# Optimization experiments

Hardware: AMD Instinct MI355X
Metric: run time of the kernel (lower is better)

## Reference

```python
import jax, jax.numpy as jnp
import numpy as np

STRIDES = (8, 16, 32, 64, 128)
NUM_CLASSES = 80
TOPK = 1000
CONF_THRESH = 0.05
NMS_THRESH = 0.6
IMG_H = IMG_W = 2048
CLASS_OFFSET = 100000.0  # > any box coordinate, makes different-class boxes disjoint


def _level_decode(cls, reg, ctn, scale, stride):
    # cls: [1,C,H,W], reg: [1,4,H,W], ctn: [1,1,H,W]
    C, H, W = cls.shape[1], cls.shape[2], cls.shape[3]
    cls = jnp.transpose(cls[0], (1, 2, 0)).reshape(-1, C)       # [HW, C]
    reg = jnp.transpose(reg[0], (1, 2, 0)).reshape(-1, 4)       # [HW, 4]
    reg = jax.nn.relu(reg * scale) * stride                      # Scale + relu + stride
    ctn = jnp.transpose(ctn[0], (1, 2, 0)).reshape(-1, 1)       # [HW, 1]
    prob = jnp.sqrt(jax.nn.sigmoid(cls) * jax.nn.sigmoid(ctn))  # [HW, C]
    scores = prob.max(axis=-1)
    labels = prob.argmax(axis=-1)
    ys, xs = jnp.meshgrid(jnp.arange(H), jnp.arange(W), indexing='ij')
    anchors = (jnp.stack([xs, ys], axis=-1).reshape(-1, 2).astype(cls.dtype) + 0.5) * stride
    if scores.shape[0] > TOPK:
        scores, idx = jax.lax.top_k(scores, TOPK)
        labels, reg, anchors = labels[idx], reg[idx], anchors[idx]
    # decode (l,t,r,b) deltas around anchor centers -> (x1,y1,x2,y2)
    boxes = jnp.concatenate([anchors - reg[:, :2], anchors + reg[:, 2:]], axis=-1)
    return scores, labels, boxes


def _nms_keep(boxes, scores, valid, thresh):
    # Sequential greedy NMS, same math as the numpy loop in RTEFCOS.nms.
    order = jnp.argsort(-jnp.where(valid, scores, -jnp.inf))
    b = boxes[order]
    v = valid[order]
    x1, y1, x2, y2 = b[:, 0], b[:, 1], b[:, 2], b[:, 3]
    areas = (x2 - x1) * (y2 - y1)
    n = b.shape[0]
    pos = jnp.arange(n)

    def body(i, keep):
        xx1 = jnp.maximum(x1[i], x1)
        yy1 = jnp.maximum(y1[i], y1)
        xx2 = jnp.minimum(x2[i], x2)
        yy2 = jnp.minimum(y2[i], y2)
        inter = jnp.maximum(1e-10, xx2 - xx1) * jnp.maximum(1e-10, yy2 - yy1)
        ovr = inter / (areas[i] + areas - inter + 1e-14)
        suppress = (ovr > thresh) & (pos > i) & keep[i]
        return keep & (~suppress)

    keep_sorted = jax.lax.fori_loop(0, n, body, v)
    return jnp.zeros(n, dtype=bool).at[order].set(keep_sorted)


def reference(cls0, reg0, ctn0, cls1, reg1, ctn1, cls2, reg2, ctn2,
              cls3, reg3, ctn3, cls4, reg4, ctn4, scales):
    levels = [(cls0, reg0, ctn0), (cls1, reg1, ctn1), (cls2, reg2, ctn2),
              (cls3, reg3, ctn3), (cls4, reg4, ctn4)]
    all_s, all_l, all_b = [], [], []
    for lv, (c, r, t) in enumerate(levels):
        s, l, b = _level_decode(c, r, t, scales[lv], STRIDES[lv])
        all_s.append(s); all_l.append(l); all_b.append(b)
    scores = jnp.concatenate(all_s)   # [M]
    labels = jnp.concatenate(all_l)   # [M]
    bboxes = jnp.concatenate(all_b)   # [M, 4]
    valid = scores >= CONF_THRESH     # conf filter as mask (static shapes)
    # class-wise NMS via coordinate-offset trick: boxes of different classes
    # never overlap, so one greedy pass == per-class greedy passes.
    boxes_off = bboxes + labels[:, None].astype(bboxes.dtype) * CLASS_OFFSET
    keep = _nms_keep(boxes_off, scores, valid, NMS_THRESH)
    bboxes = bboxes / jnp.array([IMG_W, IMG_H, IMG_W, IMG_H], dtype=bboxes.dtype)
    bboxes = jnp.clip(bboxes, 0.0, 1.0)
    return bboxes, scores, labels, keep


def setup_inputs():
    key = jax.random.key(0)
    ks = jax.random.split(key, len(STRIDES))
    inp = {}
    for lv, stride in enumerate(STRIDES):
        H = IMG_H // stride
        W = IMG_W // stride
        k1, k2, k3 = jax.random.split(ks[lv], 3)
        inp[f"cls{lv}"] = jax.random.normal(k1, (1, NUM_CLASSES, H, W), jnp.float32)
        inp[f"reg{lv}"] = jax.random.uniform(k2, (1, 4, H, W), jnp.float32)
        inp[f"ctn{lv}"] = jax.random.normal(k3, (1, 1, H, W), jnp.float32)
    inp["scales"] = jnp.ones((5,), jnp.float32)
    return inp
```

## Files before the change

### kernel.cpp

```cpp
#include <hip/hip_runtime.h>
#include <math.h>

#define TOTAL_ANCHORS 87296
#define NTOPK 87040
#define NSEL 4256
#define NWORDS 67
#define NPAD   4288
#define MAXROUNDS 4300
#define CANDMAX 8192
#define NBIN 32768
#define NSLAB 8
#define PEND_VEC 3216

__device__ __forceinline__ float sigmoidf_(float x) {
    return 1.0f / (1.0f + expf(-x));
}
__device__ __forceinline__ unsigned int f2s(float f) {
    unsigned int u = __float_as_uint(f);
    return u ^ ((u >> 31) ? 0xFFFFFFFFu : 0x80000000u);
}
__device__ __forceinline__ float s2f(unsigned int k) {
    unsigned int u = (k & 0x80000000u) ? (k ^ 0x80000000u) : ~k;
    return __uint_as_float(u);
}
__device__ __forceinline__ float f4e(const float4& v, int j) {
    return (j == 0) ? v.x : ((j == 1) ? v.y : ((j == 2) ? v.z : v.w));
}
__device__ __forceinline__ void level_of(int g, int& lv, int& base, int& W, int& stride) {
    if (g < 65536)      { lv = 0; base = 0;     W = 256; stride = 8;   }
    else if (g < 81920) { lv = 1; base = 65536; W = 128; stride = 16;  }
    else if (g < 86016) { lv = 2; base = 81920; W = 64;  stride = 32;  }
    else if (g < 87040) { lv = 3; base = 86016; W = 32;  stride = 64;  }
    else                { lv = 4; base = 87040; W = 16;  stride = 128; }
}

struct InPtrs {
    const float* cls[5];
    const float* reg[5];
    const float* ctn[5];
    const float* scales;
};

__global__ __launch_bounds__(256) void cmax_kernel(InPtrs in,
        unsigned long long* __restrict__ cmax2) {
    int t = blockIdx.x * 256 + threadIdx.x;
    int a0 = t * 4;
    if (a0 >= TOTAL_ANCHORS) return;
    int cg = blockIdx.y;
    int lv, base, W, stride;
    level_of(a0, lv, base, W, stride);
    (void)stride;
    int p0 = a0 - base;
    int HW = W * W;
    const float* cls = in.cls[lv];
    float4 ct = *(const float4*)&in.ctn[lv][p0];
    float sct0 = sigmoidf_(ct.x), sct1 = sigmoidf_(ct.y);
    float sct2 = sigmoidf_(ct.z), sct3 = sigmoidf_(ct.w);
    int c0 = cg * 8;
    unsigned long long b0 = 0ull, b1 = 0ull, b2 = 0ull, b3 = 0ull;
    #pragma unroll
    for (int k = 0; k < 8; ++k) {
        float4 v = *(const float4*)&cls[(c0 + k) * HW + p0];
        unsigned long long lbl = (unsigned long long)(255 - (c0 + k));
        unsigned long long k0 = ((unsigned long long)f2s(sqrtf(__fmul_rn(sigmoidf_(v.x), sct0))) << 32) | lbl;
        unsigned long long k1 = ((unsigned long long)f2s(sqrtf(__fmul_rn(sigmoidf_(v.y), sct1))) << 32) | lbl;
        unsigned long long k2 = ((unsigned long long)f2s(sqrtf(__fmul_rn(sigmoidf_(v.z), sct2))) << 32) | lbl;
        unsigned long long k3 = ((unsigned long long)f2s(sqrtf(__fmul_rn(sigmoidf_(v.w), sct3))) << 32) | lbl;
        b0 = (k0 > b0) ? k0 : b0;
        b1 = (k1 > b1) ? k1 : b1;
        b2 = (k2 > b2) ? k2 : b2;
        b3 = (k3 > b3) ? k3 : b3;
    }
    unsigned long long* dst = cmax2 + (size_t)cg * TOTAL_ANCHORS + a0;
    dst[0] = b0; dst[1] = b1; dst[2] = b2; dst[3] = b3;
}

__global__ __launch_bounds__(256) void decode2_kernel(InPtrs in,
        const unsigned long long* __restrict__ cmax2,
        unsigned long long* __restrict__ keys, float* __restrict__ scores,
        int* __restrict__ labels, float4* __restrict__ boxes) {
    int t = blockIdx.x * 256 + threadIdx.x;
    int g0 = t * 4;
    if (g0 >= TOTAL_ANCHORS) return;
    int lv, base, W, stride;
    level_of(g0, lv, base, W, stride);
    int p0 = g0 - base;
    int HW = W * W;
    unsigned long long mk0 = 0ull, mk1 = 0ull, mk2 = 0ull, mk3 = 0ull;
    #pragma unroll
    for (int cg = 0; cg < 10; ++cg) {
        const ulonglong2* s2 = (const ulonglong2*)(cmax2 + (size_t)cg * TOTAL_ANCHORS + g0);
        ulonglong2 va = s2[0], vb = s2[1];
        mk0 = (va.x > mk0) ? va.x : mk0;
        mk1 = (va.y > mk1) ? va.y : mk1;
        mk2 = (vb.x > mk2) ? vb.x : mk2;
        mk3 = (vb.y > mk3) ? vb.y : mk3;
    }
    unsigned long long mk[4] = {mk0, mk1, mk2, mk3};
    float scale = in.scales[lv];
    float fs = (float)stride;
    const float* rg = in.reg[lv];
    float4 rq0 = *(const float4*)&rg[0 * HW + p0];
    float4 rq1 = *(const float4*)&rg[1 * HW + p0];
    float4 rq2 = *(const float4*)&rg[2 * HW + p0];
    float4 rq3 = *(const float4*)&rg[3 * HW + p0];
    float4 sc4;
    int4 lb4;
    #pragma unroll
    for (int j = 0; j < 4; ++j) {
        int p = p0 + j;
        int x = p & (W - 1);
        int y = p / W;
        float best = s2f((unsigned int)(mk[j] >> 32));
        int lbl = 255 - (int)(mk[j] & 0xFFull);
        float r0 = __fmul_rn(fmaxf(__fmul_rn(f4e(rq0, j), scale), 0.0f), fs);
        float r1 = __fmul_rn(fmaxf(__fmul_rn(f4e(rq1, j), scale), 0.0f), fs);
        float r2 = __fmul_rn(fmaxf(__fmul_rn(f4e(rq2, j), scale), 0.0f), fs);
        float r3 = __fmul_rn(fmaxf(__fmul_rn(f4e(rq3, j), scale), 0.0f), fs);
        float ax = __fmul_rn(__fadd_rn((float)x, 0.5f), fs);
        float ay = __fmul_rn(__fadd_rn((float)y, 0.5f), fs);
        float4 b;
        b.x = __fsub_rn(ax, r0);
        b.y = __fsub_rn(ay, r1);
        b.z = __fadd_rn(ax, r2);
        b.w = __fadd_rn(ay, r3);
        boxes[g0 + j] = b;
        keys[g0 + j] = (mk[j] & 0xFFFFFFFF00000000ull)
                     | (unsigned long long)(unsigned int)(~(unsigned int)(p));
        if (j == 0) { sc4.x = best; lb4.x = lbl; }
        else if (j == 1) { sc4.y = best; lb4.y = lbl; }
        else if (j == 2) { sc4.z = best; lb4.z = lbl; }
        else { sc4.w = best; lb4.w = lbl; }
    }
    *(float4*)&scores[g0] = sc4;
    *(int4*)&labels[g0] = lb4;
}

__global__ __launch_bounds__(1024) void hist_kernel(
        const unsigned long long* __restrict__ keys,
        unsigned int* __restrict__ slab) {
    __shared__ unsigned int h[NBIN / 2];
    const int starts[NSLAB] = {0, 16384, 32768, 49152, 65536, 73728, 81920, 86016};
    const int ends[NSLAB]   = {16384, 32768, 49152, 65536, 73728, 81920, 86016, 87040};
    const int tid = threadIdx.x;
    for (int i = tid; i < NBIN / 2; i += 1024) h[i] = 0u;
    __syncthreads();
    const int s = starts[blockIdx.x], e = ends[blockIdx.x];
    for (int i = s + tid; i < e; i += 1024) {
        unsigned int bin = (unsigned int)(keys[i] >> 48) & 0x7FFFu;
        atomicAdd(&h[bin >> 1], 1u << ((bin & 1u) << 4));
    }
    __syncthreads();
    unsigned int* out = slab + blockIdx.x * (NBIN / 2);
    for (int i = tid; i < NBIN / 2; i += 1024) out[i] = h[i];
}

__global__ __launch_bounds__(1024) void select_kernel(
        const unsigned int* __restrict__ slab, unsigned int* __restrict__ thr,
        unsigned int* __restrict__ cnt) {
    const int lvl = blockIdx.x;
    const int slabS[4] = {0, 4, 6, 7};
    const int slabE[4] = {4, 6, 7, 8};
    const int tid = threadIdx.x;
    if (lvl == 0 && tid < 128) cnt[tid] = 0u;
    __shared__ unsigned int csum[1024];
    unsigned int s = 0;
    for (int sb = slabS[lvl]; sb < slabE[lvl]; ++sb) {
        const unsigned int* A = slab + sb * (NBIN / 2);
        #pragma unroll 4
        for (int w = tid * 16; w < tid * 16 + 16; ++w) {
            unsigned int v = A[w];
            s += (v & 0xFFFFu) + (v >> 16);
        }
    }
    csum[tid] = s;
    __syncthreads();
    for (int off = 1; off < 1024; off <<= 1) {
        unsigned int v = csum[tid] + ((tid + off < 1024) ? csum[tid + off] : 0u);
        __syncthreads();
        csum[tid] = v;
        __syncthreads();
    }
    unsigned int incl = csum[tid];
    unsigned int incl1 = (tid == 1023) ? 0u : csum[tid + 1];
    if (incl >= 1000u && incl1 < 1000u) {
        unsigned int running = incl1;
        for (int b = tid * 32 + 31; b >= tid * 32; --b) {
            unsigned int c = 0;
            for (int sb = slabS[lvl]; sb < slabE[lvl]; ++sb) {
                unsigned int v = slab[sb * (NBIN / 2) + (b >> 1)];
                c += (v >> ((b & 1) << 4)) & 0xFFFFu;
            }
            running += c;
            if (running >= 1000u) { thr[lvl] = (unsigned int)b; break; }
        }
    }
}

__global__ __launch_bounds__(1024) void gather_kernel(
        const unsigned long long* __restrict__ keys,
        const unsigned int* __restrict__ thr,
        unsigned long long* __restrict__ cand, unsigned int* __restrict__ cnt,
        float4* __restrict__ pendzero) {
    if (blockIdx.x < 4) {
        int z = blockIdx.x * 1024 + threadIdx.x;
        if (z < PEND_VEC) pendzero[z] = make_float4(0.f, 0.f, 0.f, 0.f);
    }
    int g = blockIdx.x * 1024 + threadIdx.x;
    int lvl;
    if (g < 65536)      lvl = 0;
    else if (g < 81920) lvl = 1;
    else if (g < 86016) lvl = 2;
    else                lvl = 3;
    unsigned long long k = keys[g];
    bool pass = (((unsigned int)(k >> 48)) & 0x7FFFu) >= thr[lvl];
    __shared__ unsigned int woff[16];
    __shared__ unsigned int base_;
    const int wave = threadIdx.x >> 6, lane = threadIdx.x & 63;
    unsigned long long m = __ballot(pass);
    if (lane == 0) woff[wave] = (unsigned int)__popcll(m);
    __syncthreads();
    if (threadIdx.x == 0) {
        unsigned int tot = 0;
        #pragma unroll
        for (int w = 0; w < 16; ++w) { unsigned int c = woff[w]; woff[w] = tot; tot += c; }
        base_ = atomicAdd(&cnt[lvl << 5], tot);
    }
    __syncthreads();
    if (pass) {
        unsigned int pos = base_ + woff[wave]
                         + (unsigned int)__popcll(m & ((1ull << lane) - 1ull));
        if (pos < CANDMAX) cand[(lvl << 13) + pos] = k;
    }
}

__global__ __launch_bounds__(1024) void finalsort_kernel(
        const unsigned long long* __restrict__ cand,
        const unsigned int* __restrict__ cnt,
        unsigned long long* __restrict__ sel) {
    const int lvl = blockIdx.x;
    const int tid = threadIdx.x;
    __shared__ unsigned long long sk[CANDMAX];
    int n = (int)cnt[lvl << 5];
    if (n > CANDMAX) n = CANDMAX;
    int P = 1024;
    while (P < n) P <<= 1;
    for (int i = tid; i < P; i += 1024)
        sk[i] = (i < n) ? cand[(lvl << 13) + i] : 0ull;
    __syncthreads();
    for (int kk = 2; kk <= P; kk <<= 1) {
        for (int j = kk >> 1; j > 0; j >>= 1) {
            for (int i = tid; i < P; i += 1024) {
                int ixj = i ^ j;
                if (ixj > i) {
                    unsigned long long a = sk[i], b = sk[ixj];
                    bool sw = ((i & kk) == 0) ? (a < b) : (a > b);
                    if (sw) { sk[i] = b; sk[ixj] = a; }
                }
            }
            __syncthreads();
        }
    }
    if (tid < 1000) sel[lvl * 1000 + tid] = sk[tid];
}

__device__ __forceinline__ int count_greater(const unsigned long long* A, int n,
                                             unsigned long long x) {
    int lo = 0, hi = n;
    while (lo < hi) { int m = (lo + hi) >> 1; if (A[m] > x) lo = m + 1; else hi = m; }
    return lo;
}
__global__ __launch_bounds__(1024) void finrank_kernel(
        const unsigned long long* __restrict__ sel,
        const float* __restrict__ scores, const int* __restrict__ labels,
        const float4* __restrict__ boxes, float* __restrict__ out,
        int* __restrict__ order, float4* __restrict__ sbox,
        float* __restrict__ sarea, int* __restrict__ svalid) {
    __shared__ unsigned long long eL[NSEL];
    __shared__ unsigned long long sk4[256];
    const int tid = threadIdx.x;
    const int blk = blockIdx.x;
    int gown = 0; float scown = 0.f; int vown = 0;
    #pragma unroll
    for (int k = 0; k < 5; ++k) {
        int pos = tid + k * 1024;
        if (pos < NSEL) {
            int g;
            if (pos < 4000) {
                int lvp = pos / 1000;
                const int offs_[4] = {0, 65536, 81920, 86016};
                unsigned long long key = sel[pos];
                unsigned int p = ~((unsigned int)(key & 0xFFFFFFFFull));
                g = offs_[lvp] + (int)p;
            } else {
                g = 87040 + (pos - 4000);
            }
            float sc = scores[g];
            int valid = (sc >= 0.05f) ? 1 : 0;
            float effs = valid ? sc : -INFINITY;
            eL[pos] = ((unsigned long long)f2s(effs) << 32) | (unsigned int)(~(unsigned int)pos);
            if (k == blk) { gown = g; scown = sc; vown = valid; }
        }
    }
    __syncthreads();
    if (tid < 256) sk4[tid] = eL[4000 + tid];
    __syncthreads();
    for (int kk = 2; kk <= 256; kk <<= 1) {
        for (int j = kk >> 1; j > 0; j >>= 1) {
            if (tid < 256) {
                int ixj = tid ^ j;
                if (ixj > tid) {
                    unsigned long long a = sk4[tid], b = sk4[ixj];
                    bool sw = ((tid & kk) == 0) ? (a < b) : (a > b);
                    if (sw) { sk4[tid] = b; sk4[ixj] = a; }
                }
            }
            __syncthreads();
        }
    }
    int pos = blk * 1024 + tid;
    if (pos < NSEL) {
        int lb = labels[gown];
        float4 bx = boxes[gown];
        const float inv = 1.0f / 2048.0f;
        float4 o4;
        o4.x = fminf(fmaxf(__fmul_rn(bx.x, inv), 0.0f), 1.0f);
        o4.y = fminf(fmaxf(__fmul_rn(bx.y, inv), 0.0f), 1.0f);
        o4.z = fminf(fmaxf(__fmul_rn(bx.z, inv), 0.0f), 1.0f);
        o4.w = fminf(fmaxf(__fmul_rn(bx.w, inv), 0.0f), 1.0f);
        *(float4*)&out[pos * 4] = o4;
        out[17024 + pos] = scown;
        out[21280 + pos] = (float)lb;
        out[25536 + pos] = 0.0f;
        float off = __fmul_rn((float)lb, 100000.0f);
        float4 eb;
        eb.x = __fadd_rn(bx.x, off); eb.y = __fadd_rn(bx.y, off);
        eb.z = __fadd_rn(bx.z, off); eb.w = __fadd_rn(bx.w, off);
        float area = __fmul_rn(__fsub_rn(eb.z, eb.x), __fsub_rn(eb.w, eb.y));
        unsigned long long x = eL[pos];
        int rank = count_greater(eL,        1000, x)
                 + count_greater(eL + 1000, 1000, x)
                 + count_greater(eL + 2000, 1000, x)
                 + count_greater(eL + 3000, 1000, x)
                 + count_greater(sk4,        256, x);
        order[rank]  = pos;
        sbox[rank]   = eb;
        sarea[rank]  = area;
        svalid[rank] = vown;
    }
}

__global__ __launch_bounds__(256) void mask_kernel(
        const float4* __restrict__ sbox, const float* __restrict__ sarea,
        const int* __restrict__ svalid,
        unsigned long long* __restrict__ maskC,
        unsigned long long* __restrict__ pend0G,
        unsigned int* __restrict__ pend1G) {
    const int colTile = blockIdx.x;
    const int tid = threadIdx.x;
    const int lane = tid & 63;
    const int rowTile = blockIdx.y * 4 + (tid >> 6);
    __shared__ float4 cb[64];
    __shared__ float ca[64];
    int col0 = colTile * 64;
    if (tid < 64) {
        int c = col0 + tid;
        if (c < NSEL) { cb[tid] = sbox[c]; ca[tid] = sarea[c]; }
        else { cb[tid] = make_float4(0.f, 0.f, 0.f, 0.f); ca[tid] = 0.f; }
    }
    __syncthreads();
    if (rowTile >= NWORDS || colTile > rowTile) return;
    int cc = col0 + lane;
    int vcol = (cc < NSEL) ? svalid[cc] : 0;
    unsigned long long unkw = __ballot(vcol != 0);
    int i = rowTile * 64 + lane;
    unsigned long long bits = 0ull;
    if (i < NSEL) {
        float4 b = sbox[i];
        float ar = sarea[i];
        for (int j = 0; j < 64; ++j) {
            float xx1 = fmaxf(b.x, cb[j].x);
            float yy1 = fmaxf(b.y, cb[j].y);
            float xx2 = fminf(b.z, cb[j].z);
            float yy2 = fminf(b.w, cb[j].w);
            float w = fmaxf(1e-10f, __fsub_rn(xx2, xx1));
            float h = fmaxf(1e-10f, __fsub_rn(yy2, yy1));
            float inter = __fmul_rn(w, h);
            float denom = __fadd_rn(__fsub_rn(__fadd_rn(ar, ca[j]), inter), 1e-14f);
            float ovr = __fdiv_rn(inter, denom);
            if (ovr > 0.6f) bits |= (1ull << j);
        }
    }
    maskC[(size_t)colTile * NPAD + i] = bits;
    if (colTile < rowTile && i < NSEL && (bits & unkw)) {
        if (colTile < 64) atomicOr(&pend0G[i], 1ull << colTile);
        else              atomicOr(&pend1G[i], 1u << (colTile - 64));
    }
}

__global__ __launch_bounds__(1024) void sweep_kernel(
        const unsigned long long* __restrict__ maskC,
        const unsigned long long* __restrict__ pend0G,
        const unsigned int* __restrict__ pend1G,
        const int* __restrict__ order, const int* __restrict__ svalid,
        float* __restrict__ out_keep) {
    const int tid = threadIdx.x;
    const int lane = tid & 63;
    const int wave = tid >> 6;
    __shared__ unsigned long long keptL[NWORDS], unkL[NWORDS];
    __shared__ unsigned long long nk[NWORDS], nkC[NWORDS], ndC[NWORDS];
    __shared__ unsigned long long cm0s;
    __shared__ unsigned int cm1s;
    __shared__ int anych;
    __shared__ int wflag[16];

    unsigned long long md[5], pend0[5];
    unsigned int pendH[5];
    #pragma unroll
    for (int k = 0; k < 5; ++k) {
        int b = wave + 16 * k;
        unsigned long long w = 0ull;
        md[k] = 0ull; pend0[k] = 0ull; pendH[k] = 0u;
        if (b < NWORDS) {
            int c = b * 64 + lane;
            int v = (c < NSEL) ? svalid[c] : 0;
            w = __ballot(v != 0);
            md[k]    = maskC[(size_t)b * NPAD + c];
            pend0[k] = pend0G[c];
            pendH[k] = pend1G[c];
            if (lane == 0) { unkL[b] = w; keptL[b] = 0ull; nk[b] = 0ull; }
        }
    }
    if (tid == 0) { cm0s = 0ull; cm1s = 0u; }
    __syncthreads();

    for (int round = 0; round < MAXROUNDS; ++round) {
        unsigned long long cm0 = cm0s;
        unsigned int cm1 = cm1s;
        #pragma unroll
        for (int k = 0; k < 5; ++k) {
            int b = wave + 16 * k;
            bool kp = false, dec = false;
            if (b < NWORDS) {
                int c = b * 64 + lane;
                unsigned long long uw = unkL[b];
                if ((uw >> lane) & 1ull) {
                    bool rem = false;
                    unsigned long long todo = pend0[k] & cm0;
                    while (todo) {
                        int w = __ffsll((long long)todo) - 1;
                        todo &= todo - 1ull;
                        unsigned long long m = maskC[(size_t)w * NPAD + c];
                        if (m & nk[w]) { rem = true; break; }
                        if ((m & unkL[w]) == 0ull) pend0[k] &= ~(1ull << w);
                    }
                    if (!rem) {
                        unsigned int todoH = pendH[k] & cm1;
                        while (todoH) {
                            int bit = __ffs(todoH) - 1;
                            todoH &= todoH - 1u;
                            int w = 64 + bit;
                            unsigned long long m = maskC[(size_t)w * NPAD + c];
                            if (m & nk[w]) { rem = true; break; }
                            if ((m & unkL[w]) == 0ull) pendH[k] &= ~(1u << bit);
                        }
                    }
                    unsigned long long below = (1ull << lane) - 1ull;
                    if (!rem && (md[k] & keptL[b] & below)) rem = true;
                    if (!rem && pend0[k] == 0ull && pendH[k] == 0u
                             && (md[k] & uw & below) == 0ull) kp = true;
                    dec = rem || kp;
                }
            }
            unsigned long long kb = __ballot(kp);
            unsigned long long db = __ballot(dec);
            if (b < NWORDS && lane == 0) { nkC[b] = kb; ndC[b] = db; }
        }
        __syncthreads();
        int any = 0;
        #pragma unroll
        for (int k = 0; k < 5; ++k) {
            int b = wave + 16 * k;
            if (b >= NWORDS) continue;
            unsigned long long db = ndC[b];
            if (lane == 0) {
                keptL[b] |= nkC[b];
                unkL[b]  &= ~db;
                nk[b]     = nkC[b];
            }
            any |= (db != 0ull) ? 1 : 0;
        }
        if (lane == 0) wflag[wave] = any;
        __syncthreads();
        if (tid == 0) {
            unsigned long long c0 = 0ull; unsigned int c1 = 0u; int a = 0;
            for (int w = 0; w < 64; ++w) if (ndC[w]) c0 |= (1ull << w);
            for (int w = 64; w < NWORDS; ++w) if (ndC[w]) c1 |= (1u << (w - 64));
            #pragma unroll
            for (int w = 0; w < 16; ++w) a |= wflag[w];
            cm0s = c0; cm1s = c1; anych = a;
        }
        __syncthreads();
        if (!anych) break;
    }

    #pragma unroll
    for (int k = 0; k < 5; ++k) {
        int b = wave + 16 * k;
        if (b >= NWORDS) continue;
        int c = b * 64 + lane;
        if (c < NSEL && ((keptL[b] >> lane) & 1ull)) out_keep[order[c]] = 1.0f;
    }
}

constexpr size_t OFF_KEYS    = 0;
constexpr size_t OFF_SCORES  = OFF_KEYS    + 698368;
constexpr size_t OFF_LABELS  = OFF_SCORES  + 349184;
constexpr size_t OFF_BOXES   = OFF_LABELS  + 349184;
constexpr size_t OFF_SEL     = OFF_BOXES   + 1396736;
constexpr size_t OFF_ORDER   = OFF_SEL     + 32000;
constexpr size_t OFF_SBOX    = OFF_ORDER   + 17024;
constexpr size_t OFF_SAREA   = OFF_SBOX    + 68096;
constexpr size_t OFF_SVALID  = OFF_SAREA   + 17024;
constexpr size_t OFF_MASK    = OFF_SVALID  + 17024;
constexpr size_t OFF_CMAX2   = OFF_MASK    + (size_t)NWORDS * NPAD * 8;
constexpr size_t OFF_CNT     = OFF_CMAX2   + 10u * 698368u;
constexpr size_t OFF_PEND0   = OFF_CNT     + 512;
constexpr size_t OFF_PEND1   = OFF_PEND0   + (size_t)NPAD * 8;
constexpr size_t OFF_THR     = OFF_PEND1   + (size_t)NPAD * 4;
constexpr size_t OFF_SLAB    = OFF_THR     + 64;
constexpr size_t OFF_CAND    = OFF_SLAB    + (size_t)NSLAB * 16384u * 4u;

extern "C" void kernel_launch(void* const* d_in, const int* in_sizes, int n_in,
                              void* d_out, int out_size, void* d_ws, size_t ws_size,
                              hipStream_t stream) {
    (void)in_sizes; (void)n_in; (void)out_size; (void)ws_size;
    InPtrs P;
    for (int lv = 0; lv < 5; ++lv) {
        P.cls[lv] = (const float*)d_in[3 * lv + 0];
        P.reg[lv] = (const float*)d_in[3 * lv + 1];
        P.ctn[lv] = (const float*)d_in[3 * lv + 2];
    }
    P.scales = (const float*)d_in[15];

    char* ws = (char*)d_ws;
    unsigned long long* keys   = (unsigned long long*)(ws + OFF_KEYS);
    float*              scores = (float*)             (ws + OFF_SCORES);
    int*                labels = (int*)               (ws + OFF_LABELS);
    float4*             boxes  = (float4*)            (ws + OFF_BOXES);
    unsigned long long* sel    = (unsigned long long*)(ws + OFF_SEL);
    int*                order  = (int*)               (ws + OFF_ORDER);
    float4*             sbox   = (float4*)            (ws + OFF_SBOX);
    float*              sarea  = (float*)             (ws + OFF_SAREA);
    int*                svalid = (int*)               (ws + OFF_SVALID);
    unsigned long long* maskb  = (unsigned long long*)(ws + OFF_MASK);
    unsigned long long* cmax2  = (unsigned long long*)(ws + OFF_CMAX2);
    unsigned int*       cnt    = (unsigned int*)      (ws + OFF_CNT);
    unsigned long long* pend0  = (unsigned long long*)(ws + OFF_PEND0);
    unsigned int*       pend1  = (unsigned int*)      (ws + OFF_PEND1);
    unsigned int*       thr    = (unsigned int*)      (ws + OFF_THR);
    unsigned int*       slab   = (unsigned int*)      (ws + OFF_SLAB);
    unsigned long long* cand   = (unsigned long long*)(ws + OFF_CAND);
    float* out = (float*)d_out;

    const int quarter_blocks = (TOTAL_ANCHORS / 4 + 255) / 256;
    cmax_kernel<<<dim3(quarter_blocks, 10), 256, 0, stream>>>(P, cmax2);
    decode2_kernel<<<quarter_blocks, 256, 0, stream>>>(P, cmax2, keys, scores, labels, boxes);
    hist_kernel<<<NSLAB, 1024, 0, stream>>>(keys, slab);
    select_kernel<<<4, 1024, 0, stream>>>(slab, thr, cnt);
    gather_kernel<<<85, 1024, 0, stream>>>(keys, thr, cand, cnt,
                                           (float4*)(ws + OFF_PEND0));
    finalsort_kernel<<<4, 1024, 0, stream>>>(cand, cnt, sel);
    finrank_kernel<<<5, 1024, 0, stream>>>(sel, scores, labels, boxes, out,
                                           order, sbox, sarea, svalid);
    mask_kernel<<<dim3(NWORDS, (NWORDS + 3) / 4), 256, 0, stream>>>(sbox, sarea, svalid,
                                                                    maskb, pend0, pend1);
    sweep_kernel<<<1, 1024, 0, stream>>>(maskb, pend0, pend1, order, svalid, out + 25536);
}
```

Measured before the change: 122.6 us.

## Fuse all pipeline stages into one persistent kernel with grid barriers

Replaces the nine-kernel launch chain with a single persistent kernel of 128 blocks. Stages are separated by atomic-counter grid barriers, plus a small kernel that zeroes the barrier counters. The aim is to remove per-launch overhead and inter-kernel gaps between many small dependent stages. The risks are deadlock if all 128 blocks are not co-resident, lower occupancy from 1024-thread blocks with 64KB of LDS during the wide cmax/decode phases, and barrier spin cost.

Measured after the change: 201.0 us. 64.0% more time.

```diff
diff --git a/kernel.cpp b/kernel.cpp
--- a/kernel.cpp
+++ b/kernel.cpp
@@ -2,6 +2,7 @@
 #include <math.h>
 
 #define TOTAL_ANCHORS 87296
+#define NQ 21824
 #define NTOPK 87040
 #define NSEL 4256
 #define NWORDS 67
@@ -11,6 +12,7 @@
 #define NBIN 32768
 #define NSLAB 8
 #define PEND_VEC 3216
+#define NB 128
 
 __device__ __forceinline__ float sigmoidf_(float x) {
     return 1.0f / (1.0f + expf(-x));
@@ -33,6 +35,12 @@
     else if (g < 87040) { lv = 3; base = 86016; W = 32;  stride = 64;  }
     else                { lv = 4; base = 87040; W = 16;  stride = 128; }
 }
+__device__ __forceinline__ int count_greater(const unsigned long long* A, int n,
+                                             unsigned long long x) {
+    int lo = 0, hi = n;
+    while (lo < hi) { int m = (lo + hi) >> 1; if (A[m] > x) lo = m + 1; else hi = m; }
+    return lo;
+}
 
 struct InPtrs {
     const float* cls[5];
@@ -40,476 +48,474 @@
     const float* ctn[5];
     const float* scales;
 };
-
-__global__ __launch_bounds__(256) void cmax_kernel(InPtrs in,
-        unsigned long long* __restrict__ cmax2) {
-    int t = blockIdx.x * 256 + threadIdx.x;
-    int a0 = t * 4;
-    if (a0 >= TOTAL_ANCHORS) return;
-    int cg = blockIdx.y;
-    int lv, base, W, stride;
-    level_of(a0, lv, base, W, stride);
-    (void)stride;
-    int p0 = a0 - base;
-    int HW = W * W;
-    const float* cls = in.cls[lv];
-    float4 ct = *(const float4*)&in.ctn[lv][p0];
-    float sct0 = sigmoidf_(ct.x), sct1 = sigmoidf_(ct.y);
-    float sct2 = sigmoidf_(ct.z), sct3 = sigmoidf_(ct.w);
-    int c0 = cg * 8;
-    unsigned long long b0 = 0ull, b1 = 0ull, b2 = 0ull, b3 = 0ull;
-    #pragma unroll
-    for (int k = 0; k < 8; ++k) {
-        float4 v = *(const float4*)&cls[(c0 + k) * HW + p0];
-        unsigned long long lbl = (unsigned long long)(255 - (c0 + k));
-        unsigned long long k0 = ((unsigned long long)f2s(sqrtf(__fmul_rn(sigmoidf_(v.x), sct0))) << 32) | lbl;
-        unsigned long long k1 = ((unsigned long long)f2s(sqrtf(__fmul_rn(sigmoidf_(v.y), sct1))) << 32) | lbl;
-        unsigned long long k2 = ((unsigned long long)f2s(sqrtf(__fmul_rn(sigmoidf_(v.z), sct2))) << 32) | lbl;
-        unsigned long long k3 = ((unsigned long long)f2s(sqrtf(__fmul_rn(sigmoidf_(v.w), sct3))) << 32) | lbl;
-        b0 = (k0 > b0) ? k0 : b0;
-        b1 = (k1 > b1) ? k1 : b1;
-        b2 = (k2 > b2) ? k2 : b2;
-        b3 = (k3 > b3) ? k3 : b3;
-    }
-    unsigned long long* dst = cmax2 + (size_t)cg * TOTAL_ANCHORS + a0;
-    dst[0] = b0; dst[1] = b1; dst[2] = b2; dst[3] = b3;
-}
-
-__global__ __launch_bounds__(256) void decode2_kernel(InPtrs in,
-        const unsigned long long* __restrict__ cmax2,
-        unsigned long long* __restrict__ keys, float* __restrict__ scores,
-        int* __restrict__ labels, float4* __restrict__ boxes) {
-    int t = blockIdx.x * 256 + threadIdx.x;
-    int g0 = t * 4;
-    if (g0 >= TOTAL_ANCHORS) return;
-    int lv, base, W, stride;
-    level_of(g0, lv, base, W, stride);
-    int p0 = g0 - base;
-    int HW = W * W;
-    unsigned long long mk0 = 0ull, mk1 = 0ull, mk2 = 0ull, mk3 = 0ull;
-    #pragma unroll
-    for (int cg = 0; cg < 10; ++cg) {
-        const ulonglong2* s2 = (const ulonglong2*)(cmax2 + (size_t)cg * TOTAL_ANCHORS + g0);
-        ulonglong2 va = s2[0], vb = s2[1];
-        mk0 = (va.x > mk0) ? va.x : mk0;
-        mk1 = (va.y > mk1) ? va.y : mk1;
-        mk2 = (vb.x > mk2) ? vb.x : mk2;
-        mk3 = (vb.y > mk3) ? vb.y : mk3;
-    }
-    unsigned long long mk[4] = {mk0, mk1, mk2, mk3};
-    float scale = in.scales[lv];
-    float fs = (float)stride;
-    const float* rg = in.reg[lv];
-    float4 rq0 = *(const float4*)&rg[0 * HW + p0];
-    float4 rq1 = *(const float4*)&rg[1 * HW + p0];
-    float4 rq2 = *(const float4*)&rg[2 * HW + p0];
-    float4 rq3 = *(const float4*)&rg[3 * HW + p0];
-    float4 sc4;
-    int4 lb4;
-    #pragma unroll
-    for (int j = 0; j < 4; ++j) {
-        int p = p0 + j;
-        int x = p & (W - 1);
-        int y = p / W;
-        float best = s2f((unsigned int)(mk[j] >> 32));
-        int lbl = 255 - (int)(mk[j] & 0xFFull);
-        float r0 = __fmul_rn(fmaxf(__fmul_rn(f4e(rq0, j), scale), 0.0f), fs);
-        float r1 = __fmul_rn(fmaxf(__fmul_rn(f4e(rq1, j), scale), 0.0f), fs);
-        float r2 = __fmul_rn(fmaxf(__fmul_rn(f4e(rq2, j), scale), 0.0f), fs);
-        float r3 = __fmul_rn(fmaxf(__fmul_rn(f4e(rq3, j), scale), 0.0f), fs);
-        float ax = __fmul_rn(__fadd_rn((float)x, 0.5f), fs);
-        float ay = __fmul_rn(__fadd_rn((float)y, 0.5f), fs);
-        float4 b;
-        b.x = __fsub_rn(ax, r0);
-        b.y = __fsub_rn(ay, r1);
-        b.z = __fadd_rn(ax, r2);
-        b.w = __fadd_rn(ay, r3);
-        boxes[g0 + j] = b;
-        keys[g0 + j] = (mk[j] & 0xFFFFFFFF00000000ull)
-                     | (unsigned long long)(unsigned int)(~(unsigned int)(p));
-        if (j == 0) { sc4.x = best; lb4.x = lbl; }
-        else if (j == 1) { sc4.y = best; lb4.y = lbl; }
-        else if (j == 2) { sc4.z = best; lb4.z = lbl; }
-        else { sc4.w = best; lb4.w = lbl; }
-    }
-    *(float4*)&scores[g0] = sc4;
-    *(int4*)&labels[g0] = lb4;
-}
-
-__global__ __launch_bounds__(1024) void hist_kernel(
-        const unsigned long long* __restrict__ keys,
-        unsigned int* __restrict__ slab) {
-    __shared__ unsigned int h[NBIN / 2];
-    const int starts[NSLAB] = {0, 16384, 32768, 49152, 65536, 73728, 81920, 86016};
-    const int ends[NSLAB]   = {16384, 32768, 49152, 65536, 73728, 81920, 86016, 87040};
-    const int tid = threadIdx.x;
-    for (int i = tid; i < NBIN / 2; i += 1024) h[i] = 0u;
-    __syncthreads();
-    const int s = starts[blockIdx.x], e = ends[blockIdx.x];
-    for (int i = s + tid; i < e; i += 1024) {
-        unsigned int bin = (unsigned int)(keys[i] >> 48) & 0x7FFFu;
-        atomicAdd(&h[bin >> 1], 1u << ((bin & 1u) << 4));
-    }
-    __syncthreads();
-    unsigned int* out = slab + blockIdx.x * (NBIN / 2);
-    for (int i = tid; i < NBIN / 2; i += 1024) out[i] = h[i];
-}
-
-__global__ __launch_bounds__(1024) void select_kernel(
-        const unsigned int* __restrict__ slab, unsigned int* __restrict__ thr,
-        unsigned int* __restrict__ cnt) {
-    const int lvl = blockIdx.x;
-    const int slabS[4] = {0, 4, 6, 7};
-    const int slabE[4] = {4, 6, 7, 8};
-    const int tid = threadIdx.x;
-    if (lvl == 0 && tid < 128) cnt[tid] = 0u;
-    __shared__ unsigned int csum[1024];
-    unsigned int s = 0;
-    for (int sb = slabS[lvl]; sb < slabE[lvl]; ++sb) {
-        const unsigned int* A = slab + sb * (NBIN / 2);
-        #pragma unroll 4
-        for (int w = tid * 16; w < tid * 16 + 16; ++w) {
-            unsigned int v = A[w];
-            s += (v & 0xFFFFu) + (v >> 16);
-        }
-    }
-    csum[tid] = s;
-    __syncthreads();
-    for (int off = 1; off < 1024; off <<= 1) {
-        unsigned int v = csum[tid] + ((tid + off < 1024) ? csum[tid + off] : 0u);
-        __syncthreads();
-        csum[tid] = v;
-        __syncthreads();
-    }
-    unsigned int incl = csum[tid];
-    unsigned int incl1 = (tid == 1023) ? 0u : csum[tid + 1];
-    if (incl >= 1000u && incl1 < 1000u) {
-        unsigned int running = incl1;
-        for (int b = tid * 32 + 31; b >= tid * 32; --b) {
-            unsigned int c = 0;
-            for (int sb = slabS[lvl]; sb < slabE[lvl]; ++sb) {
-                unsigned int v = slab[sb * (NBIN / 2) + (b >> 1)];
-                c += (v >> ((b & 1) << 4)) & 0xFFFFu;
-            }
-            running += c;
-            if (running >= 1000u) { thr[lvl] = (unsigned int)b; break; }
-        }
-    }
-}
-
-__global__ __launch_bounds__(1024) void gather_kernel(
-        const unsigned long long* __restrict__ keys,
-        const unsigned int* __restrict__ thr,
-        unsigned long long* __restrict__ cand, unsigned int* __restrict__ cnt,
-        float4* __restrict__ pendzero) {
-    if (blockIdx.x < 4) {
-        int z = blockIdx.x * 1024 + threadIdx.x;
-        if (z < PEND_VEC) pendzero[z] = make_float4(0.f, 0.f, 0.f, 0.f);
-    }
-    int g = blockIdx.x * 1024 + threadIdx.x;
-    int lvl;
-    if (g < 65536)      lvl = 0;
-    else if (g < 81920) lvl = 1;
-    else if (g < 86016) lvl = 2;
-    else                lvl = 3;
-    unsigned long long k = keys[g];
-    bool pass = (((unsigned int)(k >> 48)) & 0x7FFFu) >= thr[lvl];
-    __shared__ unsigned int woff[16];
-    __shared__ unsigned int base_;
-    const int wave = threadIdx.x >> 6, lane = threadIdx.x & 63;
-    unsigned long long m = __ballot(pass);
-    if (lane == 0) woff[wave] = (unsigned int)__popcll(m);
+struct MPtrs {
+    unsigned long long *keys, *cmax2, *cand, *sel, *maskC, *pend0G;
+    unsigned int *slab, *thr, *cnt, *pend1G, *bars;
+    float *scores, *sarea, *out;
+    int *labels, *order, *svalid;
+    float4 *boxes, *sbox;
+};
+
+__device__ __forceinline__ void gsync(unsigned int* bars, int idx) {
     __syncthreads();
     if (threadIdx.x == 0) {
-        unsigned int tot = 0;
+        __threadfence();
+        unsigned int a = atomicAdd(&bars[idx * 32], 1u) + 1u;
+        if (a < (unsigned int)NB) {
+            while (atomicAdd(&bars[idx * 32], 0u) < (unsigned int)NB)
+                __builtin_amdgcn_s_sleep(4);
+        }
+        __threadfence();
+    }
+    __syncthreads();
+}
+
+__global__ __launch_bounds__(256) void zerobars_kernel(unsigned int* bars) {
+    bars[threadIdx.x] = 0u;
+}
+
+__global__ __launch_bounds__(1024) void mega_kernel(InPtrs in, MPtrs m) {
+    __shared__ __align__(16) unsigned char smraw[65536];
+    const int tid = threadIdx.x;
+    const int bid = blockIdx.x;
+    const int gid = bid * 1024 + tid;
+
+    for (int i = gid; i < NQ * 10; i += NB * 1024) {
+        int cg = i / NQ;
+        int t = i - cg * NQ;
+        int a0 = t * 4;
+        int lv, base, W, stride;
+        level_of(a0, lv, base, W, stride);
+        (void)stride;
+        int p0 = a0 - base;
+        int HW = W * W;
+        const float* cls = in.cls[lv];
+        float4 ct = *(const float4*)&in.ctn[lv][p0];
+        float sct0 = sigmoidf_(ct.x), sct1 = sigmoidf_(ct.y);
+        float sct2 = sigmoidf_(ct.z), sct3 = sigmoidf_(ct.w);
+        int c0 = cg * 8;
+        unsigned long long b0 = 0ull, b1 = 0ull, b2 = 0ull, b3 = 0ull;
         #pragma unroll
-        for (int w = 0; w < 16; ++w) { unsigned int c = woff[w]; woff[w] = tot; tot += c; }
-        base_ = atomicAdd(&cnt[lvl << 5], tot);
-    }
-    __syncthreads();
-    if (pass) {
-        unsigned int pos = base_ + woff[wave]
-                         + (unsigned int)__popcll(m & ((1ull << lane) - 1ull));
-        if (pos < CANDMAX) cand[(lvl << 13) + pos] = k;
-    }
-}
-
-__global__ __launch_bounds__(1024) void finalsort_kernel(
-        const unsigned long long* __restrict__ cand,
-        const unsigned int* __restrict__ cnt,
-        unsigned long long* __restrict__ sel) {
-    const int lvl = blockIdx.x;
-    const int tid = threadIdx.x;
-    __shared__ unsigned long long sk[CANDMAX];
-    int n = (int)cnt[lvl << 5];
-    if (n > CANDMAX) n = CANDMAX;
-    int P = 1024;
-    while (P < n) P <<= 1;
-    for (int i = tid; i < P; i += 1024)
-        sk[i] = (i < n) ? cand[(lvl << 13) + i] : 0ull;
-    __syncthreads();
-    for (int kk = 2; kk <= P; kk <<= 1) {
-        for (int j = kk >> 1; j > 0; j >>= 1) {
-            for (int i = tid; i < P; i += 1024) {
-                int ixj = i ^ j;
-                if (ixj > i) {
-                    unsigned long long a = sk[i], b = sk[ixj];
-                    bool sw = ((i & kk) == 0) ? (a < b) : (a > b);
-                    if (sw) { sk[i] = b; sk[ixj] = a; }
-                }
-            }
+        for (int k = 0; k < 8; ++k) {
+            float4 v = *(const float4*)&cls[(c0 + k) * HW + p0];
+            unsigned long long lbl = (unsigned long long)(255 - (c0 + k));
+            unsigned long long k0 = ((unsigned long long)f2s(sqrtf(__fmul_rn(sigmoidf_(v.x), sct0))) << 32) | lbl;
+            unsigned long long k1 = ((unsigned long long)f2s(sqrtf(__fmul_rn(sigmoidf_(v.y), sct1))) << 32) | lbl;
+            unsigned long long k2 = ((unsigned long long)f2s(sqrtf(__fmul_rn(sigmoidf_(v.z), sct2))) << 32) | lbl;
+            unsigned long long k3 = ((unsigned long long)f2s(sqrtf(__fmul_rn(sigmoidf_(v.w), sct3))) << 32) | lbl;
+            b0 = (k0 > b0) ? k0 : b0;
+            b1 = (k1 > b1) ? k1 : b1;
+            b2 = (k2 > b2) ? k2 : b2;
+            b3 = (k3 > b3) ? k3 : b3;
+        }
+        unsigned long long* dst = m.cmax2 + (size_t)cg * TOTAL_ANCHORS + a0;
+        dst[0] = b0; dst[1] = b1; dst[2] = b2; dst[3] = b3;
+    }
+    if (gid < PEND_VEC) ((float4*)m.pend0G)[gid] = make_float4(0.f, 0.f, 0.f, 0.f);
+    else if (gid < PEND_VEC + 128) m.cnt[gid - PEND_VEC] = 0u;
+    gsync(m.bars, 0);
+
+    if (gid < NQ) {
+        int g0 = gid * 4;
+        int lv, base, W, stride;
+        level_of(g0, lv, base, W, stride);
+        int p0 = g0 - base;
+        int HW = W * W;
+        unsigned long long mk0 = 0ull, mk1 = 0ull, mk2 = 0ull, mk3 = 0ull;
+        #pragma unroll
+        for (int cg = 0; cg < 10; ++cg) {
+            const ulonglong2* s2 = (const ulonglong2*)(m.cmax2 + (size_t)cg * TOTAL_ANCHORS + g0);
+            ulonglong2 va = s2[0], vb = s2[1];
+            mk0 = (va.x > mk0) ? va.x : mk0;
+            mk1 = (va.y > mk1) ? va.y : mk1;
+            mk2 = (vb.x > mk2) ? vb.x : mk2;
+            mk3 = (vb.y > mk3) ? vb.y : mk3;
+        }
+        unsigned long long mk[4] = {mk0, mk1, mk2, mk3};
+        float scale = in.scales[lv];
+        float fs = (float)stride;
+        const float* rg = in.reg[lv];
+        float4 rq0 = *(const float4*)&rg[0 * HW + p0];
+        float4 rq1 = *(const float4*)&rg[1 * HW + p0];
+        float4 rq2 = *(const float4*)&rg[2 * HW + p0];
+        float4 rq3 = *(const float4*)&rg[3 * HW + p0];
+        float4 sc4; int4 lb4;
+        #pragma unroll
+        for (int j = 0; j < 4; ++j) {
+            int p = p0 + j;
+            int x = p & (W - 1);
+            int y = p / W;
+            float best = s2f((unsigned int)(mk[j] >> 32));
+            int lbl = 255 - (int)(mk[j] & 0xFFull);
+            float r0 = __fmul_rn(fmaxf(__fmul_rn(f4e(rq0, j), scale), 0.0f), fs);
+            float r1 = __fmul_rn(fmaxf(__fmul_rn(f4e(rq1, j), scale), 0.0f), fs);
+            float r2 = __fmul_rn(fmaxf(__fmul_rn(f4e(rq2, j), scale), 0.0f), fs);
+            float r3 = __fmul_rn(fmaxf(__fmul_rn(f4e(rq3, j), scale), 0.0f), fs);
+            float ax = __fmul_rn(__fadd_rn((float)x, 0.5f), fs);
+            float ay = __fmul_rn(__fadd_rn((float)y, 0.5f), fs);
+            float4 b;
+            b.x = __fsub_rn(ax, r0);
+            b.y = __fsub_rn(ay, r1);
+            b.z = __fadd_rn(ax, r2);
+            b.w = __fadd_rn(ay, r3);
+            m.boxes[g0 + j] = b;
+            m.keys[g0 + j] = (mk[j] & 0xFFFFFFFF00000000ull)
+                           | (unsigned long long)(unsigned int)(~(unsigned int)p);
+            if (j == 0) { sc4.x = best; lb4.x = lbl; }
+            else if (j == 1) { sc4.y = best; lb4.y = lbl; }
+            else if (j == 2) { sc4.z = best; lb4.z = lbl; }
+            else { sc4.w = best; lb4.w = lbl; }
+        }
+        *(float4*)&m.scores[g0] = sc4;
+        *(int4*)&m.labels[g0] = lb4;
+    }
+    gsync(m.bars, 1);
+
+    if (bid < NSLAB) {
+        unsigned int* h = (unsigned int*)smraw;
+        const int starts[NSLAB] = {0, 16384, 32768, 49152, 65536, 73728, 81920, 86016};
+        const int ends[NSLAB]   = {16384, 32768, 49152, 65536, 73728, 81920, 86016, 87040};
+        for (int i = tid; i < NBIN / 2; i += 1024) h[i] = 0u;
+        __syncthreads();
+        const int s = starts[bid], e = ends[bid];
+        for (int i = s + tid; i < e; i += 1024) {
+            unsigned int bin = (unsigned int)(m.keys[i] >> 48) & 0x7FFFu;
+            atomicAdd(&h[bin >> 1], 1u << ((bin & 1u) << 4));
+        }
+        __syncthreads();
+        unsigned int* outp = m.slab + bid * (NBIN / 2);
+        for (int i = tid; i < NBIN / 2; i += 1024) outp[i] = h[i];
+    }
+    gsync(m.bars, 2);
+
+    if (bid < 4) {
+        const int lvl = bid;
+        const int slabS[4] = {0, 4, 6, 7};
+        const int slabE[4] = {4, 6, 7, 8};
+        unsigned int* csum = (unsigned int*)smraw;
+        unsigned int s = 0;
+        for (int sb = slabS[lvl]; sb < slabE[lvl]; ++sb) {
+            const unsigned int* A = m.slab + sb * (NBIN / 2);
+            #pragma unroll 4
+            for (int w = tid * 16; w < tid * 16 + 16; ++w) {
+                unsigned int v = A[w];
+                s += (v & 0xFFFFu) + (v >> 16);
+            }
+        }
+        csum[tid] = s;
+        __syncthreads();
+        for (int off = 1; off < 1024; off <<= 1) {
+            unsigned int v = csum[tid] + ((tid + off < 1024) ? csum[tid + off] : 0u);
             __syncthreads();
-        }
-    }
-    if (tid < 1000) sel[lvl * 1000 + tid] = sk[tid];
-}
-
-__device__ __forceinline__ int count_greater(const unsigned long long* A, int n,
-                                             unsigned long long x) {
-    int lo = 0, hi = n;
-    while (lo < hi) { int m = (lo + hi) >> 1; if (A[m] > x) lo = m + 1; else hi = m; }
-    return lo;
-}
-__global__ __launch_bounds__(1024) void finrank_kernel(
-        const unsigned long long* __restrict__ sel,
-        const float* __restrict__ scores, const int* __restrict__ labels,
-        const float4* __restrict__ boxes, float* __restrict__ out,
-        int* __restrict__ order, float4* __restrict__ sbox,
-        float* __restrict__ sarea, int* __restrict__ svalid) {
-    __shared__ unsigned long long eL[NSEL];
-    __shared__ unsigned long long sk4[256];
-    const int tid = threadIdx.x;
-    const int blk = blockIdx.x;
-    int gown = 0; float scown = 0.f; int vown = 0;
-    #pragma unroll
-    for (int k = 0; k < 5; ++k) {
-        int pos = tid + k * 1024;
+            csum[tid] = v;
+            __syncthreads();
+        }
+        unsigned int incl = csum[tid];
+        unsigned int incl1 = (tid == 1023) ? 0u : csum[tid + 1];
+        if (incl >= 1000u && incl1 < 1000u) {
+            unsigned int running = incl1;
+            for (int b = tid * 32 + 31; b >= tid * 32; --b) {
+                unsigned int c = 0;
+                for (int sb = slabS[lvl]; sb < slabE[lvl]; ++sb) {
+                    unsigned int v = m.slab[sb * (NBIN / 2) + (b >> 1)];
+                    c += (v >> ((b & 1) << 4)) & 0xFFFFu;
+                }
+                running += c;
+                if (running >= 1000u) { m.thr[lvl] = (unsigned int)b; break; }
+            }
+        }
+    }
+    gsync(m.bars, 3);
+
+    if (bid < 85) {
+        unsigned int* woff = (unsigned int*)smraw;
+        int g = gid;
+        int lvl;
+        if (g < 65536)      lvl = 0;
+        else if (g < 81920) lvl = 1;
+        else if (g < 86016) lvl = 2;
+        else                lvl = 3;
+        unsigned long long k = m.keys[g];
+        bool pass = (((unsigned int)(k >> 48)) & 0x7FFFu) >= m.thr[lvl];
+        const int wave = tid >> 6, lane = tid & 63;
+        unsigned long long mm = __ballot(pass);
+        if (lane == 0) woff[wave] = (unsigned int)__popcll(mm);
+        __syncthreads();
+        if (tid == 0) {
+            unsigned int tot = 0;
+            #pragma unroll
+            for (int w = 0; w < 16; ++w) { unsigned int c = woff[w]; woff[w] = tot; tot += c; }
+            woff[16] = atomicAdd(&m.cnt[lvl << 5], tot);
+        }
+        __syncthreads();
+        if (pass) {
+            unsigned int pos = woff[16] + woff[wave]
+                             + (unsigned int)__popcll(mm & ((1ull << lane) - 1ull));
+            if (pos < CANDMAX) m.cand[(lvl << 13) + pos] = k;
+        }
+    }
+    gsync(m.bars, 4);
+
+    if (bid < 4) {
+        const int lvl = bid;
+        unsigned long long* sk = (unsigned long long*)smraw;
+        int n = (int)m.cnt[lvl << 5];
+        if (n > CANDMAX) n = CANDMAX;
+        int P = 1024;
+        while (P < n) P <<= 1;
+        for (int i = tid; i < P; i += 1024)
+            sk[i] = (i < n) ? m.cand[(lvl << 13) + i] : 0ull;
+        __syncthreads();
+        for (int kk = 2; kk <= P; kk <<= 1) {
+            for (int j = kk >> 1; j > 0; j >>= 1) {
+                for (int i = tid; i < P; i += 1024) {
+                    int ixj = i ^ j;
+                    if (ixj > i) {
+                        unsigned long long a = sk[i], b = sk[ixj];
+                        bool sw = ((i & kk) == 0) ? (a < b) : (a > b);
+                        if (sw) { sk[i] = b; sk[ixj] = a; }
+                    }
+                }
+                __syncthreads();
+            }
+        }
+        if (tid < 1000) m.sel[lvl * 1000 + tid] = sk[tid];
+    }
+    gsync(m.bars, 5);
+
+    if (bid < 5) {
+        unsigned long long* eL  = (unsigned long long*)smraw;
+        unsigned long long* sk4 = (unsigned long long*)(smraw + 34048);
+        int gown = 0; float scown = 0.f; int vown = 0;
+        #pragma unroll
+        for (int k = 0; k < 5; ++k) {
+            int pos = tid + k * 1024;
+            if (pos < NSEL) {
+                int g;
+                if (pos < 4000) {
+                    int lvp = pos / 1000;
+                    const int offs_[4] = {0, 65536, 81920, 86016};
+                    unsigned long long key = m.sel[pos];
+                    unsigned int p = ~((unsigned int)(key & 0xFFFFFFFFull));
+                    g = offs_[lvp] + (int)p;
+                } else {
+                    g = 87040 + (pos - 4000);
+                }
+                float sc = m.scores[g];
+                int valid = (sc >= 0.05f) ? 1 : 0;
+                float effs = valid ? sc : -INFINITY;
+                eL[pos] = ((unsigned long long)f2s(effs) << 32) | (unsigned int)(~(unsigned int)pos);
+                if (k == bid) { gown = g; scown = sc; vown = valid; }
+            }
+        }
+        __syncthreads();
+        if (tid < 256) sk4[tid] = eL[4000 + tid];
+        __syncthreads();
+        for (int kk = 2; kk <= 256; kk <<= 1) {
+            for (int j = kk >> 1; j > 0; j >>= 1) {
+                if (tid < 256) {
+                    int ixj = tid ^ j;
+                    if (ixj > tid) {
+                        unsigned long long a = sk4[tid], b = sk4[ixj];
+                        bool sw = ((tid & kk) == 0) ? (a < b) : (a > b);
+                        if (sw) { sk4[tid] = b; sk4[ixj] = a; }
+                    }
+                }
+                __syncthreads();
+            }
+        }
+        int pos = bid * 1024 + tid;
         if (pos < NSEL) {
-            int g;
-            if (pos < 4000) {
-                int lvp = pos / 1000;
-                const int offs_[4] = {0, 65536, 81920, 86016};
-                unsigned long long key = sel[pos];
-                unsigned int p = ~((unsigned int)(key & 0xFFFFFFFFull));
-                g = offs_[lvp] + (int)p;
-            } else {
-                g = 87040 + (pos - 4000);
-            }
-            float sc = scores[g];
-            int valid = (sc >= 0.05f) ? 1 : 0;
-            float effs = valid ? sc : -INFINITY;
-            eL[pos] = ((unsigned long long)f2s(effs) << 32) | (unsigned int)(~(unsigned int)pos);
-            if (k == blk) { gown = g; scown = sc; vown = valid; }
-        }
-    }
-    __syncthreads();
-    if (tid < 256) sk4[tid] = eL[4000 + tid];
-    __syncthreads();
-    for (int kk = 2; kk <= 256; kk <<= 1) {
-        for (int j = kk >> 1; j > 0; j >>= 1) {
-            if (tid < 256) {
-                int ixj = tid ^ j;
-                if (ixj > tid) {
-                    unsigned long long a = sk4[tid], b = sk4[ixj];
-                    bool sw = ((tid & kk) == 0) ? (a < b) : (a > b);
-                    if (sw) { sk4[tid] = b; sk4[ixj] = a; }
-                }
-            }
-            __syncthreads();
-        }
-    }
-    int pos = blk * 1024 + tid;
-    if (pos < NSEL) {
-        int lb = labels[gown];
-        float4 bx = boxes[gown];
-        const float inv = 1.0f / 2048.0f;
-        float4 o4;
-        o4.x = fminf(fmaxf(__fmul_rn(bx.x, inv), 0.0f), 1.0f);
-        o4.y = fminf(fmaxf(__fmul_rn(bx.y, inv), 0.0f), 1.0f);
-        o4.z = fminf(fmaxf(__fmul_rn(bx.z, inv), 0.0f), 1.0f);
-        o4.w = fminf(fmaxf(__fmul_rn(bx.w, inv), 0.0f), 1.0f);
-        *(float4*)&out[pos * 4] = o4;
-        out[17024 + pos] = scown;
-        out[21280 + pos] = (float)lb;
-        out[25536 + pos] = 0.0f;
-        float off = __fmul_rn((float)lb, 100000.0f);
-        float4 eb;
-        eb.x = __fadd_rn(bx.x, off); eb.y = __fadd_rn(bx.y, off);
-        eb.z = __fadd_rn(bx.z, off); eb.w = __fadd_rn(bx.w, off);
-        float area = __fmul_rn(__fsub_rn(eb.z, eb.x), __fsub_rn(eb.w, eb.y));
-        unsigned long long x = eL[pos];
-        int rank = count_greater(eL,        1000, x)
-                 + count_greater(eL + 1000, 1000, x)
-                 + count_greater(eL + 2000, 1000, x)
-                 + count_greater(eL + 3000, 1000, x)
-                 + count_greater(sk4,        256, x);
-        order[rank]  = pos;
-        sbox[rank]   = eb;
-        sarea[rank]  = area;
-        svalid[rank] = vown;
-    }
-}
-
-__global__ __launch_bounds__(256) void mask_kernel(
-        const float4* __restrict__ sbox, const float* __restrict__ sarea,
-        const int* __restrict__ svalid,
-        unsigned long long* __restrict__ maskC,
-        unsigned long long* __restrict__ pend0G,
-        unsigned int* __restrict__ pend1G) {
-    const int colTile = blockIdx.x;
-    const int tid = threadIdx.x;
-    const int lane = tid & 63;
-    const int rowTile = blockIdx.y * 4 + (tid >> 6);
-    __shared__ float4 cb[64];
-    __shared__ float ca[64];
-    int col0 = colTile * 64;
-    if (tid < 64) {
-        int c = col0 + tid;
-        if (c < NSEL) { cb[tid] = sbox[c]; ca[tid] = sarea[c]; }
-        else { cb[tid] = make_float4(0.f, 0.f, 0.f, 0.f); ca[tid] = 0.f; }
-    }
-    __syncthreads();
-    if (rowTile >= NWORDS || colTile > rowTile) return;
-    int cc = col0 + lane;
-    int vcol = (cc < NSEL) ? svalid[cc] : 0;
-    unsigned long long unkw = __ballot(vcol != 0);
-    int i = rowTile * 64 + lane;
-    unsigned long long bits = 0ull;
-    if (i < NSEL) {
-        float4 b = sbox[i];
-        float ar = sarea[i];
-        for (int j = 0; j < 64; ++j) {
-            float xx1 = fmaxf(b.x, cb[j].x);
-            float yy1 = fmaxf(b.y, cb[j].y);
-            float xx2 = fminf(b.z, cb[j].z);
-            float yy2 = fminf(b.w, cb[j].w);
-            float w = fmaxf(1e-10f, __fsub_rn(xx2, xx1));
-            float h = fmaxf(1e-10f, __fsub_rn(yy2, yy1));
-            float inter = __fmul_rn(w, h);
-            float denom = __fadd_rn(__fsub_rn(__fadd_rn(ar, ca[j]), inter), 1e-14f);
-            float ovr = __fdiv_rn(inter, denom);
-            if (ovr > 0.6f) bits |= (1ull << j);
-        }
-    }
-    maskC[(size_t)colTile * NPAD + i] = bits;
-    if (colTile < rowTile && i < NSEL && (bits & unkw)) {
-        if (colTile < 64) atomicOr(&pend0G[i], 1ull << colTile);
-        else              atomicOr(&pend1G[i], 1u << (colTile - 64));
-    }
-}
-
-__global__ __launch_bounds__(1024) void sweep_kernel(
-        const unsigned long long* __restrict__ maskC,
-        const unsigned long long* __restrict__ pend0G,
-        const unsigned int* __restrict__ pend1G,
-        const int* __restrict__ order, const int* __restrict__ svalid,
-        float* __restrict__ out_keep) {
-    const int tid = threadIdx.x;
-    const int lane = tid & 63;
-    const int wave = tid >> 6;
-    __shared__ unsigned long long keptL[NWORDS], unkL[NWORDS];
-    __shared__ unsigned long long nk[NWORDS], nkC[NWORDS], ndC[NWORDS];
-    __shared__ unsigned long long cm0s;
-    __shared__ unsigned int cm1s;
-    __shared__ int anych;
-    __shared__ int wflag[16];
-
-    unsigned long long md[5], pend0[5];
-    unsigned int pendH[5];
-    #pragma unroll
-    for (int k = 0; k < 5; ++k) {
-        int b = wave + 16 * k;
-        unsigned long long w = 0ull;
-        md[k] = 0ull; pend0[k] = 0ull; pendH[k] = 0u;
-        if (b < NWORDS) {
-            int c = b * 64 + lane;
-            int v = (c < NSEL) ? svalid[c] : 0;
-            w = __ballot(v != 0);
-            md[k]    = maskC[(size_t)b * NPAD + c];
-            pend0[k] = pend0G[c];
-            pendH[k] = pend1G[c];
-            if (lane == 0) { unkL[b] = w; keptL[b] = 0ull; nk[b] = 0ull; }
-        }
-    }
-    if (tid == 0) { cm0s = 0ull; cm1s = 0u; }
-    __syncthreads();
-
-    for (int round = 0; round < MAXROUNDS; ++round) {
-        unsigned long long cm0 = cm0s;
-        unsigned int cm1 = cm1s;
+            int lb = m.labels[gown];
+            float4 bx = m.boxes[gown];
+            const float inv = 1.0f / 2048.0f;
+            float4 o4;
+            o4.x = fminf(fmaxf(__fmul_rn(bx.x, inv), 0.0f), 1.0f);
+            o4.y = fminf(fmaxf(__fmul_rn(bx.y, inv), 0.0f), 1.0f);
+            o4.z = fminf(fmaxf(__fmul_rn(bx.z, inv), 0.0f), 1.0f);
+            o4.w = fminf(fmaxf(__fmul_rn(bx.w, inv), 0.0f), 1.0f);
+            *(float4*)&m.out[pos * 4] = o4;
+            m.out[17024 + pos] = scown;
+            m.out[21280 + pos] = (float)lb;
+            m.out[25536 + pos] = 0.0f;
+            float off = __fmul_rn((float)lb, 100000.0f);
+            float4 eb;
+            eb.x = __fadd_rn(bx.x, off); eb.y = __fadd_rn(bx.y, off);
+            eb.z = __fadd_rn(bx.z, off); eb.w = __fadd_rn(bx.w, off);
+            float area = __fmul_rn(__fsub_rn(eb.z, eb.x), __fsub_rn(eb.w, eb.y));
+            unsigned long long x = eL[pos];
+            int rank = count_greater(eL,        1000, x)
+                     + count_greater(eL + 1000, 1000, x)
+                     + count_greater(eL + 2000, 1000, x)
+                     + count_greater(eL + 3000, 1000, x)
+                     + count_greater(sk4,        256, x);
+            m.order[rank]  = pos;
+            m.sbox[rank]   = eb;
+            m.sarea[rank]  = area;
+            m.svalid[rank] = vown;
+        }
+    }
+    gsync(m.bars, 6);
+
+    {
+        float4* cbuf = (float4*)smraw;
+        float*  cav  = (float*)(smraw + 16384);
+        const int wv = tid >> 6, lane = tid & 63;
+        const int gw = bid * 16 + wv;
+        for (int t = gw; t < (NWORDS * (NWORDS + 1)) / 2; t += NB * 16) {
+            int r = (int)((sqrtf(8.0f * (float)t + 1.0f) - 1.0f) * 0.5f);
+            while ((r + 1) * (r + 2) / 2 <= t) ++r;
+            while (r * (r + 1) / 2 > t) --r;
+            int c = t - r * (r + 1) / 2;
+            int col0 = c * 64;
+            int cc = col0 + lane;
+            float4 cbx; float car; int vcol = 0;
+            if (cc < NSEL) { cbx = m.sbox[cc]; car = m.sarea[cc]; vcol = m.svalid[cc]; }
+            else { cbx = make_float4(0.f, 0.f, 0.f, 0.f); car = 0.f; }
+            cbuf[wv * 64 + lane] = cbx;
+            cav[wv * 64 + lane] = car;
+            unsigned long long unkw = __ballot(vcol != 0);
+            asm volatile("s_waitcnt lgkmcnt(0)" ::: "memory");
+            int i = r * 64 + lane;
+            unsigned long long bits = 0ull;
+            if (i < NSEL) {
+                float4 b = m.sbox[i];
+                float ar = m.sarea[i];
+                for (int j = 0; j < 64; ++j) {
+                    float4 cj = cbuf[wv * 64 + j];
+                    float caj = cav[wv * 64 + j];
+                    float xx1 = fmaxf(b.x, cj.x);
+                    float yy1 = fmaxf(b.y, cj.y);
+                    float xx2 = fminf(b.z, cj.z);
+                    float yy2 = fminf(b.w, cj.w);
+                    float w = fmaxf(1e-10f, __fsub_rn(xx2, xx1));
+                    float h = fmaxf(1e-10f, __fsub_rn(yy2, yy1));
+                    float inter = __fmul_rn(w, h);
+                    float denom = __fadd_rn(__fsub_rn(__fadd_rn(ar, caj), inter), 1e-14f);
+                    float ovr = __fdiv_rn(inter, denom);
+                    if (ovr > 0.6f) bits |= (1ull << j);
+                }
+            }
+            m.maskC[(size_t)c * NPAD + i] = bits;
+            if (c < r && i < NSEL && (bits & unkw)) {
+                if (c < 64) atomicOr(&m.pend0G[i], 1ull << c);
+                else        atomicOr(&m.pend1G[i], 1u << (c - 64));
+            }
+        }
+    }
+    gsync(m.bars, 7);
+
+    if (bid == 0) {
+        unsigned long long* keptL = (unsigned long long*)smraw;
+        unsigned long long* unkL  = keptL + 68;
+        unsigned long long* nk    = keptL + 136;
+        unsigned long long* nkC   = keptL + 204;
+        unsigned long long* ndC   = keptL + 272;
+        unsigned long long* cm0s  = keptL + 340;
+        unsigned int* cm1s = (unsigned int*)(keptL + 341);
+        int* anych = (int*)(cm1s + 1);
+        int* wflag = (int*)(cm1s + 2);
+        const int lane = tid & 63;
+        const int wave = tid >> 6;
+
+        unsigned long long md[5], pend0[5];
+        unsigned int pendH[5];
         #pragma unroll
         for (int k = 0; k < 5; ++k) {
             int b = wave + 16 * k;
-            bool kp = false, dec = false;
+            unsigned long long w = 0ull;
+            md[k] = 0ull; pend0[k] = 0ull; pendH[k] = 0u;
             if (b < NWORDS) {
                 int c = b * 64 + lane;
-                unsigned long long uw = unkL[b];
-                if ((uw >> lane) & 1ull) {
-                    bool rem = false;
-                    unsigned long long todo = pend0[k] & cm0;
-                    while (todo) {
-                        int w = __ffsll((long long)todo) - 1;
-                        todo &= todo - 1ull;
-                        unsigned long long m = maskC[(size_t)w * NPAD + c];
-                        if (m & nk[w]) { rem = true; break; }
-                        if ((m & unkL[w]) == 0ull) pend0[k] &= ~(1ull << w);
+                int v = (c < NSEL) ? m.svalid[c] : 0;
+                w = __ballot(v != 0);
+                md[k]    = m.maskC[(size_t)b * NPAD + c];
+                pend0[k] = m.pend0G[c];
+                pendH[k] = m.pend1G[c];
+                if (lane == 0) { unkL[b] = w; keptL[b] = 0ull; nk[b] = 0ull; }
+            }
+        }
+        if (tid == 0) { *cm0s = 0ull; *cm1s = 0u; }
+        __syncthreads();
+
+        for (int round = 0; round < MAXROUNDS; ++round) {
+            unsigned long long cm0 = *cm0s;
+            unsigned int cm1 = *cm1s;
+            #pragma unroll
+            for (int k = 0; k < 5; ++k) {
+                int b = wave + 16 * k;
+                bool kp = false, dec = false;
+                if (b < NWORDS) {
+                    int c = b * 64 + lane;
+                    unsigned long long uw = unkL[b];
+                    if ((uw >> lane) & 1ull) {
+                        bool rem = false;
+                        unsigned long long todo = pend0[k] & cm0;
+                        while (todo) {
+                            int w = __ffsll((long long)todo) - 1;
+                            todo &= todo - 1ull;
+                            unsigned long long mm = m.maskC[(size_t)w * NPAD + c];
+                            if (mm & nk[w]) { rem = true; break; }
+                            if ((mm & unkL[w]) == 0ull) pend0[k] &= ~(1ull << w);
+                        }
+                        if (!rem) {
+                            unsigned int todoH = pendH[k] & cm1;
+                            while (todoH) {
+                                int bit = __ffs(todoH) - 1;
+                                todoH &= todoH - 1u;
+                                int w = 64 + bit;
+                                unsigned long long mm = m.maskC[(size_t)w * NPAD + c];
+                                if (mm & nk[w]) { rem = true; break; }
+                                if ((mm & unkL[w]) == 0ull) pendH[k] &= ~(1u << bit);
+                            }
+                        }
+                        unsigned long long below = (1ull << lane) - 1ull;
+                        if (!rem && (md[k] & keptL[b] & below)) rem = true;
+                        if (!rem && pend0[k] == 0ull && pendH[k] == 0u
+                                 && (md[k] & uw & below) == 0ull) kp = true;
+                        dec = rem || kp;
                     }
-                    if (!rem) {
-                        unsigned int todoH = pendH[k] & cm1;
-                        while (todoH) {
-                            int bit = __ffs(todoH) - 1;
-                            todoH &= todoH - 1u;
-                            int w = 64 + bit;
-                            unsigned long long m = maskC[(size_t)w * NPAD + c];
-                            if (m & nk[w]) { rem = true; break; }
-                            if ((m & unkL[w]) == 0ull) pendH[k] &= ~(1u << bit);
-                        }
-                    }
-                    unsigned long long below = (1ull << lane) - 1ull;
-                    if (!rem && (md[k] & keptL[b] & below)) rem = true;
-                    if (!rem && pend0[k] == 0ull && pendH[k] == 0u
-                             && (md[k] & uw & below) == 0ull) kp = true;
-                    dec = rem || kp;
-                }
-            }
-            unsigned long long kb = __ballot(kp);
-            unsigned long long db = __ballot(dec);
-            if (b < NWORDS && lane == 0) { nkC[b] = kb; ndC[b] = db; }
-        }
-        __syncthreads();
-        int any = 0;
+                }
+                unsigned long long kb = __ballot(kp);
+                unsigned long long db = __ballot(dec);
+                if (b < NWORDS && lane == 0) { nkC[b] = kb; ndC[b] = db; }
+            }
+            __syncthreads();
+            int any = 0;
+            #pragma unroll
+            for (int k = 0; k < 5; ++k) {
+                int b = wave + 16 * k;
+                if (b >= NWORDS) continue;
+                unsigned long long db = ndC[b];
+                if (lane == 0) {
+                    keptL[b] |= nkC[b];
+                    unkL[b]  &= ~db;
+                    nk[b]     = nkC[b];
+                }
+                any |= (db != 0ull) ? 1 : 0;
+            }
+            if (lane == 0) wflag[wave] = any;
+            __syncthreads();
+            if (tid == 0) {
+                unsigned long long c0 = 0ull; unsigned int c1 = 0u; int a = 0;
+                for (int w = 0; w < 64; ++w) if (ndC[w]) c0 |= (1ull << w);
+                for (int w = 64; w < NWORDS; ++w) if (ndC[w]) c1 |= (1u << (w - 64));
+                #pragma unroll
+                for (int w = 0; w < 16; ++w) a |= wflag[w];
+                *cm0s = c0; *cm1s = c1; *anych = a;
+            }
+            __syncthreads();
+            if (!*anych) break;
+        }
+
         #pragma unroll
         for (int k = 0; k < 5; ++k) {
             int b = wave + 16 * k;
             if (b >= NWORDS) continue;
-            unsigned long long db = ndC[b];
-            if (lane == 0) {
-                keptL[b] |= nkC[b];
-                unkL[b]  &= ~db;
-                nk[b]     = nkC[b];
-            }
-            any |= (db != 0ull) ? 1 : 0;
-        }
-        if (lane == 0) wflag[wave] = any;
-        __syncthreads();
-        if (tid == 0) {
-            unsigned long long c0 = 0ull; unsigned int c1 = 0u; int a = 0;
-            for (int w = 0; w < 64; ++w) if (ndC[w]) c0 |= (1ull << w);
-            for (int w = 64; w < NWORDS; ++w) if (ndC[w]) c1 |= (1u << (w - 64));
-            #pragma unroll
-            for (int w = 0; w < 16; ++w) a |= wflag[w];
-            cm0s = c0; cm1s = c1; anych = a;
-        }
-        __syncthreads();
-        if (!anych) break;
-    }
-
-    #pragma unroll
-    for (int k = 0; k < 5; ++k) {
-        int b = wave + 16 * k;
-        if (b >= NWORDS) continue;
-        int c = b * 64 + lane;
-        if (c < NSEL && ((keptL[b] >> lane) & 1ull)) out_keep[order[c]] = 1.0f;
+            int c = b * 64 + lane;
+            if (c < NSEL && ((keptL[b] >> lane) & 1ull))
+                m.out[25536 + m.order[c]] = 1.0f;
+        }
     }
 }
 
@@ -530,6 +536,7 @@
 constexpr size_t OFF_THR     = OFF_PEND1   + (size_t)NPAD * 4;
 constexpr size_t OFF_SLAB    = OFF_THR     + 64;
 constexpr size_t OFF_CAND    = OFF_SLAB    + (size_t)NSLAB * 16384u * 4u;
+constexpr size_t OFF_BARS    = OFF_CAND    + 4u * CANDMAX * 8u;
 
 extern "C" void kernel_launch(void* const* d_in, const int* in_sizes, int n_in,
                               void* d_out, int out_size, void* d_ws, size_t ws_size,
@@ -544,36 +551,27 @@
     P.scales = (const float*)d_in[15];
 
     char* ws = (char*)d_ws;
-    unsigned long long* keys   = (unsigned long long*)(ws + OFF_KEYS);
-    float*              scores = (float*)             (ws + OFF_SCORES);
-    int*                labels = (int*)               (ws + OFF_LABELS);
-    float4*             boxes  = (float4*)            (ws + OFF_BOXES);
-    unsigned long long* sel    = (unsigned long long*)(ws + OFF_SEL);
-    int*                order  = (int*)               (ws + OFF_ORDER);
-    float4*             sbox   = (float4*)            (ws + OFF_SBOX);
-    float*              sarea  = (float*)             (ws + OFF_SAREA);
-    int*                svalid = (int*)               (ws + OFF_SVALID);
-    unsigned long long* maskb  = (unsigned long long*)(ws + OFF_MASK);
-    unsigned long long* cmax2  = (unsigned long long*)(ws + OFF_CMAX2);
-    unsigned int*       cnt    = (unsigned int*)      (ws + OFF_CNT);
-    unsigned long long* pend0  = (unsigned long long*)(ws + OFF_PEND0);
-    unsigned int*       pend1  = (unsigned int*)      (ws + OFF_PEND1);
-    unsigned int*       thr    = (unsigned int*)      (ws + OFF_THR);
-    unsigned int*       slab   = (unsigned int*)      (ws + OFF_SLAB);
-    unsigned long long* cand   = (unsigned long long*)(ws + OFF_CAND);
-    float* out = (float*)d_out;
-
-    const int quarter_blocks = (TOTAL_ANCHORS / 4 + 255) / 256;
-    cmax_kernel<<<dim3(quarter_blocks, 10), 256, 0, stream>>>(P, cmax2);
-    decode2_kernel<<<quarter_blocks, 256, 0, stream>>>(P, cmax2, keys, scores, labels, boxes);
-    hist_kernel<<<NSLAB, 1024, 0, stream>>>(keys, slab);
-    select_kernel<<<4, 1024, 0, stream>>>(slab, thr, cnt);
-    gather_kernel<<<85, 1024, 0, stream>>>(keys, thr, cand, cnt,
-                                           (float4*)(ws + OFF_PEND0));
-    finalsort_kernel<<<4, 1024, 0, stream>>>(cand, cnt, sel);
-    finrank_kernel<<<5, 1024, 0, stream>>>(sel, scores, labels, boxes, out,
-                                           order, sbox, sarea, svalid);
-    mask_kernel<<<dim3(NWORDS, (NWORDS + 3) / 4), 256, 0, stream>>>(sbox, sarea, svalid,
-                                                                    maskb, pend0, pend1);
-    sweep_kernel<<<1, 1024, 0, stream>>>(maskb, pend0, pend1, order, svalid, out + 25536);
-}
+    MPtrs M;
+    M.keys   = (unsigned long long*)(ws + OFF_KEYS);
+    M.scores = (float*)             (ws + OFF_SCORES);
+    M.labels = (int*)               (ws + OFF_LABELS);
+    M.boxes  = (float4*)            (ws + OFF_BOXES);
+    M.sel    = (unsigned long long*)(ws + OFF_SEL);
+    M.order  = (int*)               (ws + OFF_ORDER);
+    M.sbox   = (float4*)            (ws + OFF_SBOX);
+    M.sarea  = (float*)             (ws + OFF_SAREA);
+    M.svalid = (int*)               (ws + OFF_SVALID);
+    M.maskC  = (unsigned long long*)(ws + OFF_MASK);
+    M.cmax2  = (unsigned long long*)(ws + OFF_CMAX2);
+    M.cnt    = (unsigned int*)      (ws + OFF_CNT);
+    M.pend0G = (unsigned long long*)(ws + OFF_PEND0);
+    M.pend1G = (unsigned int*)      (ws + OFF_PEND1);
+    M.thr    = (unsigned int*)      (ws + OFF_THR);
+    M.slab   = (unsigned int*)      (ws + OFF_SLAB);
+    M.cand   = (unsigned long long*)(ws + OFF_CAND);
+    M.bars   = (unsigned int*)      (ws + OFF_BARS);
+    M.out    = (float*)d_out;
+
+    zerobars_kernel<<<1, 256, 0, stream>>>(M.bars);
+    mega_kernel<<<NB, 1024, 0, stream>>>(P, M);
+}
```
